# Performance work log

Hardware: AMD Instinct MI355X
Metric: run time of the kernel (lower is better)

## Reference

```python
import jax, jax.numpy as jnp
import numpy as np

N_WIRES = 3  # state vector of 2^3 = 8 amplitudes, kept as [B,2,2,2]


def _rx(t):
    c = jnp.cos(t / 2); s = jnp.sin(t / 2)
    return jnp.stack([jnp.stack([c + 0j, -1j * s], -1),
                      jnp.stack([-1j * s, c + 0j], -1)], -2).astype(jnp.complex64)


def _ry(t):
    c = jnp.cos(t / 2); s = jnp.sin(t / 2)
    return jnp.stack([jnp.stack([c, -s], -1),
                      jnp.stack([s, c], -1)], -2).astype(jnp.complex64)


def _rz(t):
    e = jnp.exp(-1j * t / 2).astype(jnp.complex64)
    z = jnp.zeros_like(e)
    return jnp.stack([jnp.stack([e, z], -1),
                      jnp.stack([z, jnp.conj(e)], -1)], -2)


def apply_1q(state, mat, wire):
    # state: [B,2,2,2]; mat: [2,2] (shared) or [B,2,2] (per-sample)
    s = jnp.moveaxis(state, 1 + wire, 1)
    sh = s.shape
    s = s.reshape(sh[0], 2, -1)
    m = jnp.broadcast_to(mat, (sh[0], 2, 2))
    s = jnp.einsum('bij,bjk->bik', m, s)
    return jnp.moveaxis(s.reshape(sh), 1, 1 + wire)


def apply_crx(state, t, ctrl, tgt):
    # controlled-RX: apply rx(t) to target subspace where control bit == 1
    mat = _rx(t)  # [2,2]
    s = jnp.moveaxis(state, (1 + ctrl, 1 + tgt), (1, 2))  # [B,2(ctrl),2(tgt),2]
    s1 = s[:, 1]                       # [B,2,2]
    sh = s1.shape
    s1 = jnp.einsum('ij,bjk->bik', mat, s1.reshape(sh[0], 2, -1)).reshape(sh)
    s = jnp.stack([s[:, 0], s1], 1)
    return jnp.moveaxis(s, (1, 2), (1 + ctrl, 1 + tgt))


def _quantum_forward(x, theta, W1, b1, W2, b2):
    B = x.shape[0]
    state = jnp.zeros((B, 2, 2, 2), jnp.complex64).at[:, 0, 0, 0].set(1.0)
    # GeneralEncoder: rx(x0)@w0, ry(x1)@w1, rz(x2)@w2
    state = apply_1q(state, _rx(x[:, 0]), 0)
    state = apply_1q(state, _ry(x[:, 1]), 1)
    state = apply_1q(state, _rz(x[:, 2]), 2)
    # RandomLayer(n_ops=8): fixed representative 8-op trainable sequence
    state = apply_1q(state, _rx(theta[0]), 0)
    state = apply_1q(state, _ry(theta[1]), 1)
    state = apply_1q(state, _rz(theta[2]), 2)
    state = apply_crx(state, theta[3], 0, 1)
    state = apply_1q(state, _ry(theta[4]), 2)
    state = apply_1q(state, _rx(theta[5]), 1)
    state = apply_crx(state, theta[6], 1, 2)
    state = apply_1q(state, _rz(theta[7]), 0)
    # measurement -> 8 basis-state probabilities (matches Linear(8,32) head)
    probs = (state.real ** 2 + state.imag ** 2).reshape(B, 8)
    h = jax.nn.relu(probs @ W1 + b1)
    return h @ W2 + b2


def setup_inputs() -> dict:
    key = jax.random.key(0)
    ks = jax.random.split(key, 6)
    B = 2_000_000
    x = jax.random.normal(ks[0], (B, 3), jnp.float32)
    theta = jax.random.normal(ks[1], (8,), jnp.float32)
    W1 = jax.random.normal(ks[2], (8, 32), jnp.float32) * 0.35   # ~1/sqrt(8)
    b1 = jnp.zeros((32,), jnp.float32)
    W2 = jax.random.normal(ks[3], (32, 2), jnp.float32) * 0.18   # ~1/sqrt(32)
    b2 = jnp.zeros((2,), jnp.float32)
    return {"x": x, "theta": theta, "W1": W1, "b1": b1, "W2": W2, "b2": b2}


def reference(x, theta, W1, b1, W2, b2):
    return _quantum_forward(x, theta, W1, b1, W2, b2)
```

## Files before the change

kernel.cpp:

```cpp
#include <hip/hip_runtime.h>


typedef float f32x2 __attribute__((ext_vector_type(2)));

static __device__ __forceinline__ f32x2 pk_fma(f32x2 a, f32x2 b, f32x2 c) {
    return __builtin_elementwise_fma(a, b, c);
}
static __device__ __forceinline__ f32x2 splat2(float v) {
    f32x2 r; r.x = v; r.y = v; return r;
}

#define INV_2PI 0.15915494309189535f

__global__ __launch_bounds__(64) void q_precompute(
    const float* __restrict__ theta,
    const float* __restrict__ W1,
    const float* __restrict__ b1,
    const float* __restrict__ W2,
    const float* __restrict__ b2,
    float* __restrict__ tab)
{
    __shared__ float Ure[8][8];
    __shared__ float Uim[8][8];
    const int t = threadIdx.x;

    if (t < 8) {
        float cr[8], ci[8];
        #pragma unroll
        for (int r = 0; r < 8; ++r) { cr[r] = (r == t) ? 1.f : 0.f; ci[r] = 0.f; }

        auto rxmix = [&](int a, int b, float c_, float s_) {
            float ar = cr[a], ai = ci[a], br = cr[b], bi = ci[b];
            cr[a] = c_*ar + s_*bi;   ci[a] = c_*ai - s_*br;
            cr[b] = s_*ai + c_*br;   ci[b] = -s_*ar + c_*bi;
        };
        auto rymix = [&](int a, int b, float c_, float s_) {
            float ar = cr[a], ai = ci[a], br = cr[b], bi = ci[b];
            cr[a] = c_*ar - s_*br;   ci[a] = c_*ai - s_*bi;
            cr[b] = s_*ar + c_*br;   ci[b] = s_*ai + c_*bi;
        };
        auto zmul = [&](int r, float u, float v) {
            float xr = cr[r], xi = ci[r];
            cr[r] = xr*u - xi*v;  ci[r] = xr*v + xi*u;
        };
        auto hsin = [&](float a) { return __builtin_amdgcn_sinf(a * (0.5f*INV_2PI)); };
        auto hcos = [&](float a) { return __builtin_amdgcn_cosf(a * (0.5f*INV_2PI)); };

        float c, s;
        c = hcos(theta[0]); s = hsin(theta[0]);
        rxmix(0,4,c,s); rxmix(1,5,c,s); rxmix(2,6,c,s); rxmix(3,7,c,s);
        c = hcos(theta[1]); s = hsin(theta[1]);
        rymix(0,2,c,s); rymix(1,3,c,s); rymix(4,6,c,s); rymix(5,7,c,s);
        c = hcos(theta[2]); s = hsin(theta[2]);
        #pragma unroll
        for (int r = 0; r < 8; ++r) zmul(r, c, (r & 1) ? s : -s);
        c = hcos(theta[3]); s = hsin(theta[3]);
        rxmix(4,6,c,s); rxmix(5,7,c,s);
        c = hcos(theta[4]); s = hsin(theta[4]);
        rymix(0,1,c,s); rymix(2,3,c,s); rymix(4,5,c,s); rymix(6,7,c,s);
        c = hcos(theta[5]); s = hsin(theta[5]);
        rxmix(0,2,c,s); rxmix(1,3,c,s); rxmix(4,6,c,s); rxmix(5,7,c,s);
        c = hcos(theta[6]); s = hsin(theta[6]);
        rxmix(2,3,c,s); rxmix(6,7,c,s);
        c = hcos(theta[7]); s = hsin(theta[7]);
        #pragma unroll
        for (int r = 0; r < 8; ++r) zmul(r, c, (r < 4) ? -s : s);

        #pragma unroll
        for (int r = 0; r < 8; ++r) { Ure[r][t] = cr[r]; Uim[r][t] = ci[r]; }
    }
    __syncthreads();

    if (t < 32) {
        float Wre[8][4], Wim[8][4];
        #pragma unroll
        for (int j = 0; j < 8; ++j) {
            Wre[j][0] =  Ure[j][0]; Wim[j][0] =  Uim[j][0];
            Wre[j][1] =  Ure[j][2]; Wim[j][1] =  Uim[j][2];
            Wre[j][2] =  Uim[j][4]; Wim[j][2] = -Ure[j][4];
            Wre[j][3] =  Uim[j][6]; Wim[j][3] = -Ure[j][6];
        }
        float Q[4][4];
        #pragma unroll
        for (int m = 0; m < 4; ++m)
            #pragma unroll
            for (int n = 0; n < 4; ++n) Q[m][n] = 0.f;
        #pragma unroll
        for (int j = 0; j < 8; ++j) {
            float w = W1[j*32 + t];
            #pragma unroll
            for (int m = 0; m < 4; ++m)
                #pragma unroll
                for (int n = 0; n < 4; ++n)
                    Q[m][n] = fmaf(w, Wre[j][m]*Wre[j][n] + Wim[j][m]*Wim[j][n], Q[m][n]);
        }
        float R[3][3];
        R[0][0] = Q[0][0];
        R[0][1] = Q[0][1] + Q[1][0];
        R[0][2] = Q[1][1];
        R[1][0] = Q[0][2] + Q[2][0];
        R[1][1] = Q[0][3] + Q[1][2] + Q[2][1] + Q[3][0];
        R[1][2] = Q[1][3] + Q[3][1];
        R[2][0] = Q[2][2];
        R[2][1] = Q[2][3] + Q[3][2];
        R[2][2] = Q[3][3];
        float P[3][3];
        #pragma unroll
        for (int b = 0; b < 3; ++b) {
            P[0][b] = 0.5f*(R[0][b] + R[2][b]);
            P[1][b] = 0.5f*(R[0][b] - R[2][b]);
            P[2][b] = 0.5f*R[1][b];
        }
        float T[3][3];
        #pragma unroll
        for (int si = 0; si < 3; ++si) {
            T[si][0] = 0.5f*(P[si][0] + P[si][2]);
            T[si][1] = 0.5f*(P[si][0] - P[si][2]);
            T[si][2] = 0.5f*P[si][1];
        }
        float* row = tab + t*12;
        row[0] = T[0][1]; row[1] = T[0][2]; row[2] = T[1][0]; row[3] = T[2][0];
        row[4] = T[1][1]; row[5] = T[1][2]; row[6] = T[2][1]; row[7] = T[2][2];
        row[8] = b1[t] + T[0][0];
        row[9]  = W2[t*2+0];
        row[10] = W2[t*2+1];
        row[11] = 0.f;
    }
    if (t == 0) { tab[384] = b2[0]; tab[385] = b2[1]; tab[386] = 0.f; tab[387] = 0.f; }
}

__global__ __launch_bounds__(256) void q_main(
    const float* __restrict__ x,
    const float* __restrict__ tab,
    float* __restrict__ out,
    int B)
{
    const int lid = threadIdx.x;
    const int bb  = blockIdx.x * 2048;
    const int e0  = bb + lid;

    const float b2a = tab[384], b2b = tab[385];
    const float4* T4 = (const float4*)tab;

    if (bb + 2048 <= B) {
        float xs0[8], xs1[8];
        #pragma unroll
        for (int k = 0; k < 8; ++k) {
            const int e = e0 + k*256;
            xs0[k] = x[e*3 + 0];
            xs1[k] = x[e*3 + 1];
        }

        f32x2 c0v[4], s0v[4], c1v[4], s1v[4], pcc[4], pcs[4], psc[4], pss[4];
        #pragma unroll
        for (int g = 0; g < 4; ++g) {
            #pragma unroll
            for (int j = 0; j < 2; ++j) {
                const int k = 2*g + j;
                const float r0 = xs0[k] * INV_2PI;
                const float r1 = xs1[k] * INV_2PI;
                s0v[g][j] = __builtin_amdgcn_sinf(r0);
                c0v[g][j] = __builtin_amdgcn_cosf(r0);
                s1v[g][j] = __builtin_amdgcn_sinf(r1);
                c1v[g][j] = __builtin_amdgcn_cosf(r1);
            }
            pcc[g] = c0v[g]*c1v[g]; pcs[g] = c0v[g]*s1v[g];
            psc[g] = s0v[g]*c1v[g]; pss[g] = s0v[g]*s1v[g];
        }

        f32x2 a0v[4], a1v[4];
        #pragma unroll
        for (int g = 0; g < 4; ++g) { a0v[g] = splat2(b2a); a1v[g] = splat2(b2b); }

        #pragma unroll 4
        for (int l = 0; l < 32; ++l) {
            const float4 cA = T4[l*3+0];
            const float4 cB = T4[l*3+1];
            const float4 cC = T4[l*3+2];
            #pragma unroll
            for (int g = 0; g < 4; ++g) {
                f32x2 h = pk_fma(splat2(cA.x), c1v[g], splat2(cC.x));
                h = pk_fma(splat2(cA.y), s1v[g], h);
                h = pk_fma(splat2(cA.z), c0v[g], h);
                h = pk_fma(splat2(cA.w), s0v[g], h);
                h = pk_fma(splat2(cB.x), pcc[g], h);
                h = pk_fma(splat2(cB.y), pcs[g], h);
                h = pk_fma(splat2(cB.z), psc[g], h);
                h = pk_fma(splat2(cB.w), pss[g], h);
                h = __builtin_elementwise_max(h, splat2(0.f));
                a0v[g] = pk_fma(h, splat2(cC.y), a0v[g]);
                a1v[g] = pk_fma(h, splat2(cC.z), a1v[g]);
            }
        }

        f32x2* O2 = (f32x2*)out;
        #pragma unroll
        for (int k = 0; k < 8; ++k) {
            const int e = e0 + k*256;
            f32x2 o; o.x = a0v[k>>1][k&1]; o.y = a1v[k>>1][k&1];
            O2[e] = o;
        }
    } else {
        for (int k = 0; k < 8; ++k) {
            const int e = e0 + k*256;
            if (e >= B) continue;
            const float r0 = x[e*3+0] * INV_2PI;
            const float r1 = x[e*3+1] * INV_2PI;
            const float s0 = __builtin_amdgcn_sinf(r0), c0 = __builtin_amdgcn_cosf(r0);
            const float s1 = __builtin_amdgcn_sinf(r1), c1 = __builtin_amdgcn_cosf(r1);
            const float pc = c0*c1, ps = c0*s1, sc = s0*c1, ss = s0*s1;
            float A0 = b2a, A1 = b2b;
            for (int l = 0; l < 32; ++l) {
                const float4 cA = T4[l*3+0];
                const float4 cB = T4[l*3+1];
                const float4 cC = T4[l*3+2];
                float h = cC.x;
                h = fmaf(cA.x, c1, h);
                h = fmaf(cA.y, s1, h);
                h = fmaf(cA.z, c0, h);
                h = fmaf(cA.w, s0, h);
                h = fmaf(cB.x, pc, h);
                h = fmaf(cB.y, ps, h);
                h = fmaf(cB.z, sc, h);
                h = fmaf(cB.w, ss, h);
                h = fmaxf(h, 0.f);
                A0 = fmaf(h, cC.y, A0);
                A1 = fmaf(h, cC.z, A1);
            }
            out[e*2+0] = A0;
            out[e*2+1] = A1;
        }
    }
}

extern "C" void kernel_launch(void* const* d_in, const int* in_sizes, int n_in,
                              void* d_out, int out_size, void* d_ws, size_t ws_size,
                              hipStream_t stream) {
    const float* x     = (const float*)d_in[0];
    const float* theta = (const float*)d_in[1];
    const float* W1    = (const float*)d_in[2];
    const float* b1    = (const float*)d_in[3];
    const float* W2    = (const float*)d_in[4];
    const float* b2    = (const float*)d_in[5];
    float* out = (float*)d_out;
    float* tab = (float*)d_ws;

    const int B = in_sizes[0] / 3;

    q_precompute<<<1, 64, 0, stream>>>(theta, W1, b1, W2, b2, tab);

    const int blocks = (B + 2047) / 2048;
    q_main<<<blocks, 256, 0, stream>>>(x, tab, out, B);
}
```

Before: 97.44 us.

## Fuse table precompute into main kernel with LDS table and inline packed asm

Merges the single-block precompute kernel into the main kernel. Each block now rebuilds the 8x8 unitary and the per-neuron coefficient table in shared memory, which removes a second launch and the global workspace round trip. It also forces v_pk_fma/v_pk_mul through inline asm, hoists the splatted constants, clamps tail indices instead of using a separate scalar tail path, and changes the unroll and launch bounds. The cost is that every block repeats the small precompute serially before its main work starts.

```diff
diff --git a/kernel.cpp b/kernel.cpp
--- a/kernel.cpp
+++ b/kernel.cpp
@@ -3,8 +3,15 @@
 
 typedef float f32x2 __attribute__((ext_vector_type(2)));
 
-static __device__ __forceinline__ f32x2 pk_fma(f32x2 a, f32x2 b, f32x2 c) {
-    return __builtin_elementwise_fma(a, b, c);
+static __device__ __forceinline__ f32x2 pkfma(f32x2 a, f32x2 b, f32x2 c) {
+    f32x2 d;
+    asm("v_pk_fma_f32 %0, %1, %2, %3" : "=v"(d) : "v"(a), "v"(b), "v"(c));
+    return d;
+}
+static __device__ __forceinline__ f32x2 pkmul(f32x2 a, f32x2 b) {
+    f32x2 d;
+    asm("v_pk_mul_f32 %0, %1, %2" : "=v"(d) : "v"(a), "v"(b));
+    return d;
 }
 static __device__ __forceinline__ f32x2 splat2(float v) {
     f32x2 r; r.x = v; r.y = v; return r;
@@ -12,16 +19,20 @@
 
 #define INV_2PI 0.15915494309189535f
 
-__global__ __launch_bounds__(64) void q_precompute(
+__global__ __launch_bounds__(256, 2) void q_fused(
+    const float* __restrict__ x,
     const float* __restrict__ theta,
     const float* __restrict__ W1,
     const float* __restrict__ b1,
     const float* __restrict__ W2,
     const float* __restrict__ b2,
-    float* __restrict__ tab)
+    float* __restrict__ out,
+    int B)
 {
     __shared__ float Ure[8][8];
     __shared__ float Uim[8][8];
+    __shared__ __align__(16) float tab[400];
+
     const int t = threadIdx.x;
 
     if (t < 8) {
@@ -127,108 +138,81 @@
         row[11] = 0.f;
     }
     if (t == 0) { tab[384] = b2[0]; tab[385] = b2[1]; tab[386] = 0.f; tab[387] = 0.f; }
-}
-
-__global__ __launch_bounds__(256) void q_main(
-    const float* __restrict__ x,
-    const float* __restrict__ tab,
-    float* __restrict__ out,
-    int B)
-{
+    __syncthreads();
+
     const int lid = threadIdx.x;
     const int bb  = blockIdx.x * 2048;
     const int e0  = bb + lid;
 
     const float b2a = tab[384], b2b = tab[385];
-    const float4* T4 = (const float4*)tab;
-
-    if (bb + 2048 <= B) {
-        float xs0[8], xs1[8];
-        #pragma unroll
-        for (int k = 0; k < 8; ++k) {
-            const int e = e0 + k*256;
-            xs0[k] = x[e*3 + 0];
-            xs1[k] = x[e*3 + 1];
-        }
-
-        f32x2 c0v[4], s0v[4], c1v[4], s1v[4], pcc[4], pcs[4], psc[4], pss[4];
+    const float4* T4 = reinterpret_cast<const float4*>(tab);
+
+    float xs0[8], xs1[8];
+    #pragma unroll
+    for (int k = 0; k < 8; ++k) {
+        int e = e0 + k*256;
+        e = (e < B) ? e : (B - 1);
+        xs0[k] = x[e*3 + 0];
+        xs1[k] = x[e*3 + 1];
+    }
+
+    f32x2 c0v[4], s0v[4], c1v[4], s1v[4], pcc[4], pcs[4], psc[4], pss[4];
+    #pragma unroll
+    for (int g = 0; g < 4; ++g) {
+        #pragma unroll
+        for (int j = 0; j < 2; ++j) {
+            const int k = 2*g + j;
+            const float r0 = xs0[k] * INV_2PI;
+            const float r1 = xs1[k] * INV_2PI;
+            s0v[g][j] = __builtin_amdgcn_sinf(r0);
+            c0v[g][j] = __builtin_amdgcn_cosf(r0);
+            s1v[g][j] = __builtin_amdgcn_sinf(r1);
+            c1v[g][j] = __builtin_amdgcn_cosf(r1);
+        }
+        pcc[g] = pkmul(c0v[g], c1v[g]);
+        pcs[g] = pkmul(c0v[g], s1v[g]);
+        psc[g] = pkmul(s0v[g], c1v[g]);
+        pss[g] = pkmul(s0v[g], s1v[g]);
+    }
+
+    f32x2 a0v[4], a1v[4];
+    #pragma unroll
+    for (int g = 0; g < 4; ++g) { a0v[g] = splat2(b2a); a1v[g] = splat2(b2b); }
+
+    #pragma unroll 2
+    for (int l = 0; l < 32; ++l) {
+        const float4 cA = T4[l*3+0];
+        const float4 cB = T4[l*3+1];
+        const float4 cC = T4[l*3+2];
+        const f32x2 vb  = splat2(cC.x);
+        const f32x2 vA0 = splat2(cA.x), vA1 = splat2(cA.y);
+        const f32x2 vA2 = splat2(cA.z), vA3 = splat2(cA.w);
+        const f32x2 vB0 = splat2(cB.x), vB1 = splat2(cB.y);
+        const f32x2 vB2 = splat2(cB.z), vB3 = splat2(cB.w);
+        const f32x2 vw0 = splat2(cC.y), vw1 = splat2(cC.z);
         #pragma unroll
         for (int g = 0; g < 4; ++g) {
-            #pragma unroll
-            for (int j = 0; j < 2; ++j) {
-                const int k = 2*g + j;
-                const float r0 = xs0[k] * INV_2PI;
-                const float r1 = xs1[k] * INV_2PI;
-                s0v[g][j] = __builtin_amdgcn_sinf(r0);
-                c0v[g][j] = __builtin_amdgcn_cosf(r0);
-                s1v[g][j] = __builtin_amdgcn_sinf(r1);
-                c1v[g][j] = __builtin_amdgcn_cosf(r1);
-            }
-            pcc[g] = c0v[g]*c1v[g]; pcs[g] = c0v[g]*s1v[g];
-            psc[g] = s0v[g]*c1v[g]; pss[g] = s0v[g]*s1v[g];
-        }
-
-        f32x2 a0v[4], a1v[4];
-        #pragma unroll
-        for (int g = 0; g < 4; ++g) { a0v[g] = splat2(b2a); a1v[g] = splat2(b2b); }
-
-        #pragma unroll 4
-        for (int l = 0; l < 32; ++l) {
-            const float4 cA = T4[l*3+0];
-            const float4 cB = T4[l*3+1];
-            const float4 cC = T4[l*3+2];
-            #pragma unroll
-            for (int g = 0; g < 4; ++g) {
-                f32x2 h = pk_fma(splat2(cA.x), c1v[g], splat2(cC.x));
-                h = pk_fma(splat2(cA.y), s1v[g], h);
-                h = pk_fma(splat2(cA.z), c0v[g], h);
-                h = pk_fma(splat2(cA.w), s0v[g], h);
-                h = pk_fma(splat2(cB.x), pcc[g], h);
-                h = pk_fma(splat2(cB.y), pcs[g], h);
-                h = pk_fma(splat2(cB.z), psc[g], h);
-                h = pk_fma(splat2(cB.w), pss[g], h);
-                h = __builtin_elementwise_max(h, splat2(0.f));
-                a0v[g] = pk_fma(h, splat2(cC.y), a0v[g]);
-                a1v[g] = pk_fma(h, splat2(cC.z), a1v[g]);
-            }
-        }
-
-        f32x2* O2 = (f32x2*)out;
-        #pragma unroll
-        for (int k = 0; k < 8; ++k) {
-            const int e = e0 + k*256;
+            f32x2 h = pkfma(vA0, c1v[g], vb);
+            h = pkfma(vA1, s1v[g], h);
+            h = pkfma(vA2, c0v[g], h);
+            h = pkfma(vA3, s0v[g], h);
+            h = pkfma(vB0, pcc[g], h);
+            h = pkfma(vB1, pcs[g], h);
+            h = pkfma(vB2, psc[g], h);
+            h = pkfma(vB3, pss[g], h);
+            h = __builtin_elementwise_max(h, splat2(0.f));
+            a0v[g] = pkfma(h, vw0, a0v[g]);
+            a1v[g] = pkfma(h, vw1, a1v[g]);
+        }
+    }
+
+    f32x2* O2 = (f32x2*)out;
+    #pragma unroll
+    for (int k = 0; k < 8; ++k) {
+        const int e = e0 + k*256;
+        if (e < B) {
             f32x2 o; o.x = a0v[k>>1][k&1]; o.y = a1v[k>>1][k&1];
             O2[e] = o;
-        }
-    } else {
-        for (int k = 0; k < 8; ++k) {
-            const int e = e0 + k*256;
-            if (e >= B) continue;
-            const float r0 = x[e*3+0] * INV_2PI;
-            const float r1 = x[e*3+1] * INV_2PI;
-            const float s0 = __builtin_amdgcn_sinf(r0), c0 = __builtin_amdgcn_cosf(r0);
-            const float s1 = __builtin_amdgcn_sinf(r1), c1 = __builtin_amdgcn_cosf(r1);
-            const float pc = c0*c1, ps = c0*s1, sc = s0*c1, ss = s0*s1;
-            float A0 = b2a, A1 = b2b;
-            for (int l = 0; l < 32; ++l) {
-                const float4 cA = T4[l*3+0];
-                const float4 cB = T4[l*3+1];
-                const float4 cC = T4[l*3+2];
-                float h = cC.x;
-                h = fmaf(cA.x, c1, h);
-                h = fmaf(cA.y, s1, h);
-                h = fmaf(cA.z, c0, h);
-                h = fmaf(cA.w, s0, h);
-                h = fmaf(cB.x, pc, h);
-                h = fmaf(cB.y, ps, h);
-                h = fmaf(cB.z, sc, h);
-                h = fmaf(cB.w, ss, h);
-                h = fmaxf(h, 0.f);
-                A0 = fmaf(h, cC.y, A0);
-                A1 = fmaf(h, cC.z, A1);
-            }
-            out[e*2+0] = A0;
-            out[e*2+1] = A1;
         }
     }
 }
@@ -243,12 +227,9 @@
     const float* W2    = (const float*)d_in[4];
     const float* b2    = (const float*)d_in[5];
     float* out = (float*)d_out;
-    float* tab = (float*)d_ws;
+    (void)d_ws; (void)ws_size;
 
     const int B = in_sizes[0] / 3;
-
-    q_precompute<<<1, 64, 0, stream>>>(theta, W1, b1, W2, b2, tab);
-
     const int blocks = (B + 2047) / 2048;
-    q_main<<<blocks, 256, 0, stream>>>(x, tab, out, B);
-}
+    q_fused<<<blocks, 256, 0, stream>>>(x, theta, W1, b1, W2, b2, out, B);
+}
```

Measured after the change: 100.9 us. 1.04x slower.
